# Performance work log

Hardware: AMD Instinct MI355X
Metric: run time of the kernel (lower is better)

## Reference

```python
import jax, jax.numpy as jnp
import numpy as np

# dims: G groups, A authors/group, P posts/author, DIN token-pooled feat, DEMB sentence-BERT dim
G, A, P, DIN, DEMB, HP, HA = 16, 64, 32, 768, 384, 256, 128


def setup_inputs() -> dict:
    key = jax.random.key(0)
    ks = jax.random.split(key, 8)
    s = lambda k, shape, scale: (jax.random.normal(k, shape, jnp.float32) * scale)
    return {
        "x": jax.random.normal(ks[0], (G, A, P, DIN), jnp.float32),
        "w_embed": s(ks[1], (DIN, DEMB), 0.02),   # BERT pooled-projection stand-in
        "b_embed": jnp.zeros((DEMB,), jnp.float32),
        "k_post": s(ks[2], (DEMB, 4 * HP), 0.05),  # Keras LSTM kernel, gates [i|f|c|o]
        "r_post": s(ks[3], (HP, 4 * HP), 0.05),    # recurrent kernel
        "b_post": jnp.zeros((4 * HP,), jnp.float32),
        "k_auth": s(ks[4], (HP, 4 * HA), 0.05),
        "r_auth": s(ks[5], (HA, 4 * HA), 0.05),
        "b_auth": jnp.zeros((4 * HA,), jnp.float32),
    }


def _lstm(x, Wk, Wr, b):
    """Keras-style LSTM, returns final hidden state. x: [B,T,D] -> [B,H]."""
    B = x.shape[0]
    H = Wr.shape[0]
    # precompute input projections for all timesteps in one GEMM: [T,B,4H]
    z = jnp.einsum('btd,dh->tbh', x, Wk) + b

    def step(carry, zt):
        h, c = carry
        g = zt + h @ Wr
        i, f, gg, o = jnp.split(g, 4, axis=-1)  # Keras gate order i,f,c,o
        c = jax.nn.sigmoid(f) * c + jax.nn.sigmoid(i) * jnp.tanh(gg)
        h = jax.nn.sigmoid(o) * jnp.tanh(c)
        return (h, c), None

    h0 = jnp.zeros((B, H), x.dtype)
    (h, _), _ = jax.lax.scan(step, (h0, h0), z)
    return h


def reference(x, w_embed, b_embed, k_post, r_post, b_post, k_auth, r_auth, b_auth):
    g, a, p, _ = x.shape
    # sentence embedding per post (BERT stand-in): [G,A,P,DEMB]
    e = jnp.einsum('gapd,de->gape', x, w_embed) + b_embed
    # LSTM over posts, batched across all (group, author) pairs: [G,A,HP]
    h_post = _lstm(e.reshape(g * a, p, e.shape[-1]), k_post, r_post, b_post)
    h_post = h_post.reshape(g, a, -1)
    # LSTM over authors: [G,HA]
    return _lstm(h_post, k_auth, r_auth, b_auth)
```

## Files before the change

### kernel.cpp

```cpp
#include <hip/hip_runtime.h>
#include <cstdint>
#include <cstddef>

#define G_    16
#define A_    64
#define P_    32
#define DIN_  768
#define DEMB_ 384
#define HP_   256
#define HA_   128
#define GA_   1024
#define N1_   1024
#define N2_   512
#define TCH   16

typedef float    f32x4   __attribute__((ext_vector_type(4)));
typedef _Float16 half8_t __attribute__((ext_vector_type(8)));
typedef _Float16 half4_t __attribute__((ext_vector_type(4)));

__device__ __forceinline__ float sigmoidf_(float x) { return 1.0f / (1.0f + __expf(-x)); }
__device__ __forceinline__ float tanhf_(float x) { return 2.0f / (1.0f + __expf(-2.0f * x)) - 1.0f; }
__device__ __forceinline__ _Float16 us2h(unsigned short u) { _Float16 h; __builtin_memcpy(&h, &u, 2); return h; }
__device__ __forceinline__ unsigned short h2us(_Float16 h) { unsigned short u; __builtin_memcpy(&u, &h, 2); return u; }


__global__ __launch_bounds__(256) void k_wk(const float* __restrict__ w_embed,
                                            const float* __restrict__ k_post,
                                            float* __restrict__ Bmat) {
    int j  = blockIdx.x * 256 + threadIdx.x;
    int k0 = blockIdx.y * 4;
    float acc0 = 0.f, acc1 = 0.f, acc2 = 0.f, acc3 = 0.f;
    for (int d = 0; d < DEMB_; ++d) {
        float kp = k_post[(size_t)d * N1_ + j];
        acc0 += w_embed[(size_t)(k0 + 0) * DEMB_ + d] * kp;
        acc1 += w_embed[(size_t)(k0 + 1) * DEMB_ + d] * kp;
        acc2 += w_embed[(size_t)(k0 + 2) * DEMB_ + d] * kp;
        acc3 += w_embed[(size_t)(k0 + 3) * DEMB_ + d] * kp;
    }
    Bmat[(size_t)(k0 + 0) * N1_ + j] = acc0;
    Bmat[(size_t)(k0 + 1) * N1_ + j] = acc1;
    Bmat[(size_t)(k0 + 2) * N1_ + j] = acc2;
    Bmat[(size_t)(k0 + 3) * N1_ + j] = acc3;
}

__global__ __launch_bounds__(256) void k_bias_p(const float* __restrict__ b_embed,
                                                const float* __restrict__ k_post,
                                                const float* __restrict__ b_post,
                                                float* __restrict__ biasZp) {
    int p = blockIdx.x * 256 + threadIdx.x;
    int n = (p >> 6) * 16 + (p & 15) + 256 * ((p >> 4) & 3);
    float acc = b_post[n];
    for (int d = 0; d < DEMB_; ++d)
        acc += b_embed[d] * k_post[(size_t)d * N1_ + n];
    biasZp[p] = acc;
}

__global__ __launch_bounds__(256) void k_t16(const float* __restrict__ Bmat,
                                             _Float16* __restrict__ Bt16) {
    __shared__ float tile[64][65];
    const int tid = threadIdx.x;
    const int p0 = blockIdx.x * 64;
    const int k0 = blockIdx.y * 64;
    const int jgrp = p0 >> 6;
#pragma unroll
    for (int i = 0; i < 16; ++i) {
        int idx = i * 256 + tid;
        int pp = idx & 63, kk = idx >> 6;
        int n = jgrp * 16 + (pp & 15) + 256 * ((pp >> 4) & 3);
        tile[pp][kk] = Bmat[(size_t)(k0 + kk) * N1_ + n];
    }
    __syncthreads();
    const int pp = tid >> 2;
    const int kq = (tid & 3) * 16;
    _Float16 buf[16];
#pragma unroll
    for (int i = 0; i < 16; ++i) buf[i] = (_Float16)tile[pp][kq + i];
    _Float16* dst = &Bt16[(size_t)(p0 + pp) * DIN_ + k0 + kq];
    *(half8_t*)dst       = *(half8_t*)&buf[0];
    *(half8_t*)(dst + 8) = *(half8_t*)&buf[8];
}

__global__ __launch_bounds__(256) void k_bfrag(const float* __restrict__ r_post,
                                               _Float16* __restrict__ Bfrag) {
    int idx = blockIdx.x * 256 + threadIdx.x;
    int pt = idx >> 9;
    int kt = (idx >> 6) & 7;
    int l  = idx & 63;
    int p = pt * 16 + (l & 15);
    int n = (p >> 6) * 16 + (p & 15) + 256 * ((p >> 4) & 3);
    int kb = kt * 32 + (l >> 4) * 8;
    _Float16 buf[8];
#pragma unroll
    for (int s = 0; s < 8; ++s) buf[s] = (_Float16)r_post[(size_t)(kb + s) * N1_ + n];
    *(half8_t*)&Bfrag[(size_t)idx * 8] = *(half8_t*)buf;
}

#define ZBM 128
#define ZBN 256
#define ZBK 32
#define ZPAD 40

__global__ __launch_bounds__(512, 2) void k_zgemm(const float* __restrict__ x,
                                                  const _Float16* __restrict__ Bt16,
                                                  const float* __restrict__ biasZp,
                                                  _Float16* __restrict__ Zq, int tbase) {
    __shared__ union {
        struct { _Float16 As[ZBM][ZPAD], Bs[ZBN][ZPAD]; } S;
        _Float16 Hs[64][264];
    } u;

    const int bid = blockIdx.x;
    const int wg  = (bid & 7) * 64 + (bid >> 3);
    const int bm  = (wg & 127) * ZBM;
    const int bn  = (wg >> 7) * ZBN;
    const int tid = threadIdx.x;

    const int arow = tid >> 2, akq = (tid & 3) * 8;
    const int brow = tid >> 1, bkq = (tid & 1) * 16;
    const int lane = tid & 63, w = tid >> 6;
    const int wm = (w >> 2) * 64, wn = (w & 3) * 64;
    const int frc = lane & 15, frk = (lane >> 4) * 8;

    const int crow = bm + arow;
    const size_t xrow = (size_t)(crow >> 4) * P_ + tbase + (crow & 15);
    const float*    aptr = &x[xrow * DIN_ + akq];
    const _Float16* bptr = &Bt16[(size_t)(bn + brow) * DIN_ + bkq];

    f32x4 acc[4][4];
#pragma unroll
    for (int i = 0; i < 4; ++i)
#pragma unroll
        for (int j = 0; j < 4; ++j) acc[i][j] = (f32x4)0.0f;

    float4 a0 = *(const float4*)aptr;
    float4 a1 = *(const float4*)(aptr + 4);
    uint4  b0 = *(const uint4*)bptr;
    uint4  b1 = *(const uint4*)(bptr + 8);

    const int NK = DIN_ / ZBK;
    for (int kt = 0; kt < NK; ++kt) {
        const int kn = (kt + 1 < NK) ? (kt + 1) * ZBK : kt * ZBK;
        float4 na0 = *(const float4*)(aptr + kn);
        float4 na1 = *(const float4*)(aptr + kn + 4);
        uint4  nb0 = *(const uint4*)(bptr + kn);
        uint4  nb1 = *(const uint4*)(bptr + kn + 8);

        half8_t ahv;
        {
            float av[8] = {a0.x,a0.y,a0.z,a0.w,a1.x,a1.y,a1.z,a1.w};
#pragma unroll
            for (int i = 0; i < 8; ++i) ahv[i] = (_Float16)av[i];
        }

        __syncthreads();
        *(half8_t*)&u.S.As[arow][akq]  = ahv;
        *(uint4*)&u.S.Bs[brow][bkq]     = b0;
        *(uint4*)&u.S.Bs[brow][bkq + 8] = b1;
        __syncthreads();

        half8_t bf[4];
#pragma unroll
        for (int fn = 0; fn < 4; ++fn)
            bf[fn] = *(const half8_t*)&u.S.Bs[wn + fn * 16 + frc][frk];
#pragma unroll
        for (int fm = 0; fm < 4; ++fm) {
            half8_t aH = *(const half8_t*)&u.S.As[wm + fm * 16 + frc][frk];
#pragma unroll
            for (int fn = 0; fn < 4; ++fn)
                acc[fm][fn] = __builtin_amdgcn_mfma_f32_16x16x32_f16(aH, bf[fn], acc[fm][fn], 0, 0, 0);
        }
        a0 = na0; a1 = na1; b0 = nb0; b1 = nb1;
    }

    float bzv[4];
#pragma unroll
    for (int fn = 0; fn < 4; ++fn) bzv[fn] = biasZp[bn + wn + fn * 16 + frc];

#pragma unroll
    for (int half_ = 0; half_ < 2; ++half_) {
        __syncthreads();
        if ((w >> 2) == half_) {
#pragma unroll
            for (int fm = 0; fm < 4; ++fm)
#pragma unroll
                for (int fn = 0; fn < 4; ++fn)
#pragma unroll
                    for (int r = 0; r < 4; ++r) {
                        int rl = fm * 16 + (lane >> 4) * 4 + r;
                        int cl = wn + fn * 16 + frc;
                        int clp = ((cl >> 6) * 16 + (cl & 15)) * 4 + ((cl >> 4) & 3);
                        u.Hs[rl][clp] = (_Float16)(acc[fm][fn][r] + bzv[fn]);
                    }
        }
        __syncthreads();
        const int brb = (bm + half_ * 64) >> 4;
        const int rg  = brb >> 4;
        const int l4r = (brb & 15) >> 2;
#pragma unroll
        for (int it = 0; it < 2; ++it) {
            int unit = it * 512 + tid;
            int tloc = unit >> 6, hcl = unit & 63;
            _Float16 buf[16];
#pragma unroll
            for (int rr = 0; rr < 4; ++rr) {
                half4_t h4 = *(const half4_t*)&u.Hs[tloc + 16 * rr][hcl * 4];
                buf[rr * 4 + 0] = h4[0]; buf[rr * 4 + 1] = h4[1];
                buf[rr * 4 + 2] = h4[2]; buf[rr * 4 + 3] = h4[3];
            }
            int wvg  = (bn >> 6) + (hcl >> 4);
            int tid2 = wvg * 64 + l4r * 16 + (hcl & 15);
            _Float16* dst = &Zq[((size_t)(tloc * 64 + rg) * 1024 + tid2) * 16];
            *(uint4*)dst       = *(const uint4*)&buf[0];
            *(uint4*)(dst + 8) = *(const uint4*)&buf[8];
        }
    }
}

__global__ __launch_bounds__(1024, 4) void k_rec(const _Float16* __restrict__ Zq,
                                                 const _Float16* __restrict__ Bfrag,
                                                 float* __restrict__ csave,
                                                 unsigned short* __restrict__ hsave,
                                                 float* __restrict__ hF32, int tbase) {
    __shared__ __align__(16) _Float16 wlds[16 * 8 * 64 * 8];
    __shared__ __align__(16) _Float16 hbuf[2][4096];

    const int tid = threadIdx.x, lane = tid & 63, wv = tid >> 6;
    const int hl = lane & 15, l4 = lane >> 4;
    const int r0 = blockIdx.x * 16;
    const int hc = wv * 16 + hl;

    half8_t wreg[16];
#pragma unroll
    for (int q = 0; q < 2; ++q)
#pragma unroll
        for (int kt = 0; kt < 8; ++kt)
            wreg[q * 8 + kt] = *(const half8_t*)&Bfrag[(((size_t)(4 * wv + q) * 8 + kt) * 64 + lane) * 8];
#pragma unroll
    for (int kt = 0; kt < 8; ++kt)
        *(half8_t*)&wlds[((wv * 8 + kt) * 64 + lane) * 8] =
            *(const half8_t*)&Bfrag[(((size_t)(4 * wv + 2) * 8 + kt) * 64 + lane) * 8];
    const _Float16* w3base = &Bfrag[((size_t)(4 * wv + 3) * 8 * 64 + lane) * 8];

    float cst[4];
    if (tbase == 0) {
#pragma unroll
        for (int i = 0; i < 4; ++i) cst[i] = 0.f;
    } else {
        f32x4 cv = *(const f32x4*)&csave[((size_t)blockIdx.x * 1024 + tid) * 4];
#pragma unroll
        for (int i = 0; i < 4; ++i) cst[i] = cv[i];
#pragma unroll
        for (int rr = 0; rr < 4; ++rr) {
            int row = l4 * 4 + rr;
            int lidx = (((hc >> 5) * 64) + (((hc & 31) >> 3) * 16 + row)) * 8 + (hc & 7);
            hbuf[0][lidx] = us2h(hsave[((size_t)(r0 + row)) * HP_ + hc]);
        }
    }
    __syncthreads();

    const _Float16* zp0 = &Zq[((size_t)blockIdx.x * 1024 + tid) * 16];
    half8_t z01N = *(const half8_t*)zp0;
    half8_t z23N = *(const half8_t*)(zp0 + 8);

    for (int tt = 0; tt < TCH; ++tt) {
        const int t = tbase + tt;
        const int cur = t & 1, nxt = cur ^ 1;

        half8_t z01 = z01N, z23 = z23N;
        if (tt + 1 < TCH) {
            const _Float16* zpn = zp0 + (size_t)(tt + 1) * 1048576;
            z01N = *(const half8_t*)zpn;
            z23N = *(const half8_t*)(zpn + 8);
        }

        f32x4 acc[4];
#pragma unroll
        for (int i = 0; i < 4; ++i) acc[i] = (f32x4)0.0f;

        if (t > 0) {
#pragma unroll
            for (int kt = 0; kt < 8; ++kt) {
                half8_t ah = *(const half8_t*)&hbuf[cur][(kt * 64 + lane) * 8];
                half8_t b2 = *(const half8_t*)&wlds[((wv * 8 + kt) * 64 + lane) * 8];
                half8_t w3 = *(const half8_t*)&w3base[(size_t)kt * 512];
                acc[0] = __builtin_amdgcn_mfma_f32_16x16x32_f16(ah, wreg[kt],     acc[0], 0, 0, 0);
                acc[1] = __builtin_amdgcn_mfma_f32_16x16x32_f16(ah, wreg[8 + kt], acc[1], 0, 0, 0);
                acc[2] = __builtin_amdgcn_mfma_f32_16x16x32_f16(ah, b2,           acc[2], 0, 0, 0);
                acc[3] = __builtin_amdgcn_mfma_f32_16x16x32_f16(ah, w3,           acc[3], 0, 0, 0);
            }
        }

        const bool last = (t == P_ - 1);
        const bool save = (tbase == 0) && (tt == TCH - 1);
#pragma unroll
        for (int rr = 0; rr < 4; ++rr) {
            const half8_t zsrc = (rr < 2) ? z01 : z23;
            const int o = (rr & 1) * 4;
            float gi = acc[0][rr] + (float)zsrc[o + 0];
            float gf = acc[1][rr] + (float)zsrc[o + 1];
            float gg = acc[2][rr] + (float)zsrc[o + 2];
            float go = acc[3][rr] + (float)zsrc[o + 3];
            float cn = sigmoidf_(gf) * cst[rr] + sigmoidf_(gi) * tanhf_(gg);
            cst[rr] = cn;
            float hv = sigmoidf_(go) * tanhf_(cn);
            int row = l4 * 4 + rr;
            int lidx = (((hc >> 5) * 64) + (((hc & 31) >> 3) * 16 + row)) * 8 + (hc & 7);
            _Float16 hh = (_Float16)hv;
            hbuf[nxt][lidx] = hh;
            if (save) hsave[((size_t)(r0 + row)) * HP_ + hc] = h2us(hh);
            if (last) hF32[(size_t)(r0 + row) * HP_ + hc] = hv;
        }
        __syncthreads();
    }

    if (tbase == 0) {
        f32x4 cv;
#pragma unroll
        for (int i = 0; i < 4; ++i) cv[i] = cst[i];
        *(f32x4*)&csave[((size_t)blockIdx.x * 1024 + tid) * 4] = cv;
    }
}

__global__ __launch_bounds__(256) void k_zauth(const float* __restrict__ h,
                                               const float* __restrict__ k_auth,
                                               const float* __restrict__ b_auth,
                                               float* __restrict__ z_auth) {
    const int j = blockIdx.x * 256 + threadIdx.x;
    const int r0 = blockIdx.y * 4;
    float acc0 = b_auth[j], acc1 = acc0, acc2 = acc0, acc3 = acc0;
    for (int k = 0; k < HP_; ++k) {
        const float kp = k_auth[(size_t)k * N2_ + j];
        acc0 += h[(size_t)(r0 + 0) * HP_ + k] * kp;
        acc1 += h[(size_t)(r0 + 1) * HP_ + k] * kp;
        acc2 += h[(size_t)(r0 + 2) * HP_ + k] * kp;
        acc3 += h[(size_t)(r0 + 3) * HP_ + k] * kp;
    }
#pragma unroll
    for (int r = 0; r < 4; ++r) {
        const int b = r0 + r;
        const int g = b >> 6, a = b & 63;
        const float v = (r == 0) ? acc0 : (r == 1) ? acc1 : (r == 2) ? acc2 : acc3;
        z_auth[((size_t)a * G_ + g) * N2_ + j] = v;
    }
}

__global__ __launch_bounds__(512, 2) void k_author(const float* __restrict__ z_auth,
                                                   const float* __restrict__ r_auth,
                                                   float* __restrict__ out) {
    const int g = blockIdx.x;
    const int tid = threadIdx.x;

    __shared__ float hs[HA_];
    __shared__ float gs[N2_];

    float rc[HA_];
#pragma unroll
    for (int k = 0; k < HA_; ++k)
        rc[k] = r_auth[(size_t)k * N2_ + tid];

    float cj = 0.f;
    if (tid < HA_) hs[tid] = 0.f;
    __syncthreads();

    float zn = z_auth[(size_t)g * N2_ + tid];
    for (int a = 0; a < A_; ++a) {
        float acc0 = zn, acc1 = 0.f, acc2 = 0.f, acc3 = 0.f;
        if (a + 1 < A_) zn = z_auth[((size_t)(a + 1) * G_ + g) * N2_ + tid];
#pragma unroll
        for (int k = 0; k < HA_; k += 4) {
            float4 h4 = *(const float4*)&hs[k];
            acc0 += h4.x * rc[k];
            acc1 += h4.y * rc[k + 1];
            acc2 += h4.z * rc[k + 2];
            acc3 += h4.w * rc[k + 3];
        }
        gs[tid] = (acc0 + acc1) + (acc2 + acc3);
        __syncthreads();
        if (tid < HA_) {
            const float i_ = sigmoidf_(gs[tid]);
            const float f_ = sigmoidf_(gs[tid + 128]);
            const float gg = gs[tid + 256];
            const float o_ = sigmoidf_(gs[tid + 384]);
            cj = f_ * cj + i_ * tanhf_(gg);
            hs[tid] = o_ * tanhf_(cj);
        }
        __syncthreads();
    }
    if (tid < HA_) out[(size_t)g * HA_ + tid] = hs[tid];
}

extern "C" void kernel_launch(void* const* d_in, const int* in_sizes, int n_in,
                              void* d_out, int out_size, void* d_ws, size_t ws_size,
                              hipStream_t stream) {
    const float* x       = (const float*)d_in[0];
    const float* w_embed = (const float*)d_in[1];
    const float* b_embed = (const float*)d_in[2];
    const float* k_post  = (const float*)d_in[3];
    const float* r_post  = (const float*)d_in[4];
    const float* b_post  = (const float*)d_in[5];
    const float* k_auth  = (const float*)d_in[6];
    const float* r_auth  = (const float*)d_in[7];
    const float* b_auth  = (const float*)d_in[8];
    float* out = (float*)d_out;

    char* wsb = (char*)d_ws;
    _Float16*       Zq     = (_Float16*)(wsb);
    float*          Bmat   = (float*)(wsb + (32ull << 20));
    _Float16*       Bt16   = (_Float16*)(wsb + (36ull << 20));
    _Float16*       Bfrag  = (_Float16*)(wsb + (38ull << 20));
    float*          biasZp = (float*)(wsb + (38ull << 20) + (512ull << 10));
    float*          csave  = (float*)(wsb + (39ull << 20));
    unsigned short* hsave  = (unsigned short*)(wsb + (40ull << 20));
    float*          hF32   = (float*)(wsb + (41ull << 20));
    float*          z_auth = (float*)(wsb + (42ull << 20));

    k_wk    <<<dim3(N1_ / 256, DIN_ / 4), 256, 0, stream>>>(w_embed, k_post, Bmat);
    k_bias_p<<<dim3(N1_ / 256), 256, 0, stream>>>(b_embed, k_post, b_post, biasZp);
    k_t16   <<<dim3(16, 12), 256, 0, stream>>>(Bmat, Bt16);
    k_bfrag <<<dim3(128), 256, 0, stream>>>(r_post, Bfrag);

    for (int ch = 0; ch < 2; ++ch) {
        k_zgemm<<<dim3(512), 512, 0, stream>>>(x, Bt16, biasZp, Zq, ch * TCH);
        k_rec  <<<dim3(64), 1024, 0, stream>>>(Zq, Bfrag, csave, hsave, hF32, ch * TCH);
    }

    k_zauth <<<dim3(N2_ / 256, GA_ / 4), 256, 0, stream>>>(hF32, k_auth, b_auth, z_auth);
    k_author<<<dim3(G_), 512, 0, stream>>>(z_auth, r_auth, out);
}
```

Baseline: 406.3 us.

## Overlap second-chunk input GEMM with first-chunk recurrence in fused launch

```diff
diff --git a/kernel.cpp b/kernel.cpp
--- a/kernel.cpp
+++ b/kernel.cpp
@@ -100,25 +100,30 @@
 #define ZBK 32
 #define ZPAD 40
 
-__global__ __launch_bounds__(512, 2) void k_zgemm(const float* __restrict__ x,
-                                                  const _Float16* __restrict__ Bt16,
-                                                  const float* __restrict__ biasZp,
-                                                  _Float16* __restrict__ Zq, int tbase) {
-    __shared__ union {
-        struct { _Float16 As[ZBM][ZPAD], Bs[ZBN][ZPAD]; } S;
+struct ZgLDS {
+    union {
+        struct { _Float16 As[ZBM][ZPAD]; _Float16 Bs[ZBN][ZPAD]; } S;
         _Float16 Hs[64][264];
     } u;
-
-    const int bid = blockIdx.x;
-    const int wg  = (bid & 7) * 64 + (bid >> 3);
-    const int bm  = (wg & 127) * ZBM;
-    const int bn  = (wg >> 7) * ZBN;
-    const int tid = threadIdx.x;
-
-    const int arow = tid >> 2, akq = (tid & 3) * 8;
-    const int brow = tid >> 1, bkq = (tid & 1) * 16;
+};
+struct RecLDS {
+    _Float16 wlds[16 * 8 * 64 * 8];
+    _Float16 hbuf[2][4096];
+};
+
+__device__ __forceinline__ void zgemm_core(ZgLDS* L, int bid, int tid,
+                                           const float* __restrict__ x,
+                                           const _Float16* __restrict__ Bt16,
+                                           const float* __restrict__ biasZp,
+                                           _Float16* __restrict__ Zq, int tbase) {
+    const int wg = (bid & 7) * 64 + (bid >> 3);
+    const int bm = (wg & 127) * ZBM;
+    const int bn = (wg >> 7) * ZBN;
+
+    const int arow = tid >> 3, akq = (tid & 7) * 4;
+    const int brow = tid >> 2, bkq = (tid & 3) * 8;
     const int lane = tid & 63, w = tid >> 6;
-    const int wm = (w >> 2) * 64, wn = (w & 3) * 64;
+    const int wm = (w >> 2) * 32, wn = (w & 3) * 64;
     const int frc = lane & 15, frk = (lane >> 4) * 8;
 
     const int crow = bm + arow;
@@ -126,50 +131,42 @@
     const float*    aptr = &x[xrow * DIN_ + akq];
     const _Float16* bptr = &Bt16[(size_t)(bn + brow) * DIN_ + bkq];
 
-    f32x4 acc[4][4];
-#pragma unroll
-    for (int i = 0; i < 4; ++i)
+    f32x4 acc[2][4];
+#pragma unroll
+    for (int i = 0; i < 2; ++i)
 #pragma unroll
         for (int j = 0; j < 4; ++j) acc[i][j] = (f32x4)0.0f;
 
     float4 a0 = *(const float4*)aptr;
-    float4 a1 = *(const float4*)(aptr + 4);
     uint4  b0 = *(const uint4*)bptr;
-    uint4  b1 = *(const uint4*)(bptr + 8);
 
     const int NK = DIN_ / ZBK;
     for (int kt = 0; kt < NK; ++kt) {
         const int kn = (kt + 1 < NK) ? (kt + 1) * ZBK : kt * ZBK;
         float4 na0 = *(const float4*)(aptr + kn);
-        float4 na1 = *(const float4*)(aptr + kn + 4);
         uint4  nb0 = *(const uint4*)(bptr + kn);
-        uint4  nb1 = *(const uint4*)(bptr + kn + 8);
-
-        half8_t ahv;
-        {
-            float av[8] = {a0.x,a0.y,a0.z,a0.w,a1.x,a1.y,a1.z,a1.w};
-#pragma unroll
-            for (int i = 0; i < 8; ++i) ahv[i] = (_Float16)av[i];
-        }
-
-        __syncthreads();
-        *(half8_t*)&u.S.As[arow][akq]  = ahv;
-        *(uint4*)&u.S.Bs[brow][bkq]     = b0;
-        *(uint4*)&u.S.Bs[brow][bkq + 8] = b1;
+
+        half4_t ahv;
+        ahv[0] = (_Float16)a0.x; ahv[1] = (_Float16)a0.y;
+        ahv[2] = (_Float16)a0.z; ahv[3] = (_Float16)a0.w;
+
+        __syncthreads();
+        *(half4_t*)&L->u.S.As[arow][akq] = ahv;
+        *(uint4*)&L->u.S.Bs[brow][bkq]   = b0;
         __syncthreads();
 
         half8_t bf[4];
 #pragma unroll
         for (int fn = 0; fn < 4; ++fn)
-            bf[fn] = *(const half8_t*)&u.S.Bs[wn + fn * 16 + frc][frk];
-#pragma unroll
-        for (int fm = 0; fm < 4; ++fm) {
-            half8_t aH = *(const half8_t*)&u.S.As[wm + fm * 16 + frc][frk];
+            bf[fn] = *(const half8_t*)&L->u.S.Bs[wn + fn * 16 + frc][frk];
+#pragma unroll
+        for (int fm = 0; fm < 2; ++fm) {
+            half8_t aH = *(const half8_t*)&L->u.S.As[wm + fm * 16 + frc][frk];
 #pragma unroll
             for (int fn = 0; fn < 4; ++fn)
                 acc[fm][fn] = __builtin_amdgcn_mfma_f32_16x16x32_f16(aH, bf[fn], acc[fm][fn], 0, 0, 0);
         }
-        a0 = na0; a1 = na1; b0 = nb0; b1 = nb1;
+        a0 = na0; b0 = nb0;
     }
 
     float bzv[4];
@@ -179,31 +176,29 @@
 #pragma unroll
     for (int half_ = 0; half_ < 2; ++half_) {
         __syncthreads();
-        if ((w >> 2) == half_) {
-#pragma unroll
-            for (int fm = 0; fm < 4; ++fm)
+        if ((w >> 3) == half_) {
+#pragma unroll
+            for (int fm = 0; fm < 2; ++fm)
 #pragma unroll
                 for (int fn = 0; fn < 4; ++fn)
 #pragma unroll
                     for (int r = 0; r < 4; ++r) {
-                        int rl = fm * 16 + (lane >> 4) * 4 + r;
+                        int rl = ((w >> 2) & 1) * 32 + fm * 16 + (lane >> 4) * 4 + r;
                         int cl = wn + fn * 16 + frc;
                         int clp = ((cl >> 6) * 16 + (cl & 15)) * 4 + ((cl >> 4) & 3);
-                        u.Hs[rl][clp] = (_Float16)(acc[fm][fn][r] + bzv[fn]);
+                        L->u.Hs[rl][clp] = (_Float16)(acc[fm][fn][r] + bzv[fn]);
                     }
         }
         __syncthreads();
         const int brb = (bm + half_ * 64) >> 4;
         const int rg  = brb >> 4;
         const int l4r = (brb & 15) >> 2;
-#pragma unroll
-        for (int it = 0; it < 2; ++it) {
-            int unit = it * 512 + tid;
-            int tloc = unit >> 6, hcl = unit & 63;
+        {
+            int tloc = tid >> 6, hcl = tid & 63;
             _Float16 buf[16];
 #pragma unroll
             for (int rr = 0; rr < 4; ++rr) {
-                half4_t h4 = *(const half4_t*)&u.Hs[tloc + 16 * rr][hcl * 4];
+                half4_t h4 = *(const half4_t*)&L->u.Hs[tloc + 16 * rr][hcl * 4];
                 buf[rr * 4 + 0] = h4[0]; buf[rr * 4 + 1] = h4[1];
                 buf[rr * 4 + 2] = h4[2]; buf[rr * 4 + 3] = h4[3];
             }
@@ -216,17 +211,15 @@
     }
 }
 
-__global__ __launch_bounds__(1024, 4) void k_rec(const _Float16* __restrict__ Zq,
-                                                 const _Float16* __restrict__ Bfrag,
-                                                 float* __restrict__ csave,
-                                                 unsigned short* __restrict__ hsave,
-                                                 float* __restrict__ hF32, int tbase) {
-    __shared__ __align__(16) _Float16 wlds[16 * 8 * 64 * 8];
-    __shared__ __align__(16) _Float16 hbuf[2][4096];
-
-    const int tid = threadIdx.x, lane = tid & 63, wv = tid >> 6;
+__device__ __forceinline__ void rec_core(RecLDS* L, int blk, int tid,
+                                         const _Float16* __restrict__ Zq,
+                                         const _Float16* __restrict__ Bfrag,
+                                         float* __restrict__ csave,
+                                         unsigned short* __restrict__ hsave,
+                                         float* __restrict__ hF32, int tbase) {
+    const int lane = tid & 63, wv = tid >> 6;
     const int hl = lane & 15, l4 = lane >> 4;
-    const int r0 = blockIdx.x * 16;
+    const int r0 = blk * 16;
     const int hc = wv * 16 + hl;
 
     half8_t wreg[16];
@@ -237,7 +230,7 @@
             wreg[q * 8 + kt] = *(const half8_t*)&Bfrag[(((size_t)(4 * wv + q) * 8 + kt) * 64 + lane) * 8];
 #pragma unroll
     for (int kt = 0; kt < 8; ++kt)
-        *(half8_t*)&wlds[((wv * 8 + kt) * 64 + lane) * 8] =
+        *(half8_t*)&L->wlds[((wv * 8 + kt) * 64 + lane) * 8] =
             *(const half8_t*)&Bfrag[(((size_t)(4 * wv + 2) * 8 + kt) * 64 + lane) * 8];
     const _Float16* w3base = &Bfrag[((size_t)(4 * wv + 3) * 8 * 64 + lane) * 8];
 
@@ -246,19 +239,19 @@
 #pragma unroll
         for (int i = 0; i < 4; ++i) cst[i] = 0.f;
     } else {
-        f32x4 cv = *(const f32x4*)&csave[((size_t)blockIdx.x * 1024 + tid) * 4];
+        f32x4 cv = *(const f32x4*)&csave[((size_t)blk * 1024 + tid) * 4];
 #pragma unroll
         for (int i = 0; i < 4; ++i) cst[i] = cv[i];
 #pragma unroll
         for (int rr = 0; rr < 4; ++rr) {
             int row = l4 * 4 + rr;
             int lidx = (((hc >> 5) * 64) + (((hc & 31) >> 3) * 16 + row)) * 8 + (hc & 7);
-            hbuf[0][lidx] = us2h(hsave[((size_t)(r0 + row)) * HP_ + hc]);
+            L->hbuf[0][lidx] = us2h(hsave[((size_t)(r0 + row)) * HP_ + hc]);
         }
     }
     __syncthreads();
 
-    const _Float16* zp0 = &Zq[((size_t)blockIdx.x * 1024 + tid) * 16];
+    const _Float16* zp0 = &Zq[((size_t)blk * 1024 + tid) * 16];
     half8_t z01N = *(const half8_t*)zp0;
     half8_t z23N = *(const half8_t*)(zp0 + 8);
 
@@ -280,8 +273,8 @@
         if (t > 0) {
 #pragma unroll
             for (int kt = 0; kt < 8; ++kt) {
-                half8_t ah = *(const half8_t*)&hbuf[cur][(kt * 64 + lane) * 8];
-                half8_t b2 = *(const half8_t*)&wlds[((wv * 8 + kt) * 64 + lane) * 8];
+                half8_t ah = *(const half8_t*)&L->hbuf[cur][(kt * 64 + lane) * 8];
+                half8_t b2 = *(const half8_t*)&L->wlds[((wv * 8 + kt) * 64 + lane) * 8];
                 half8_t w3 = *(const half8_t*)&w3base[(size_t)kt * 512];
                 acc[0] = __builtin_amdgcn_mfma_f32_16x16x32_f16(ah, wreg[kt],     acc[0], 0, 0, 0);
                 acc[1] = __builtin_amdgcn_mfma_f32_16x16x32_f16(ah, wreg[8 + kt], acc[1], 0, 0, 0);
@@ -306,7 +299,7 @@
             int row = l4 * 4 + rr;
             int lidx = (((hc >> 5) * 64) + (((hc & 31) >> 3) * 16 + row)) * 8 + (hc & 7);
             _Float16 hh = (_Float16)hv;
-            hbuf[nxt][lidx] = hh;
+            L->hbuf[nxt][lidx] = hh;
             if (save) hsave[((size_t)(r0 + row)) * HP_ + hc] = h2us(hh);
             if (last) hF32[(size_t)(r0 + row) * HP_ + hc] = hv;
         }
@@ -317,8 +310,41 @@
         f32x4 cv;
 #pragma unroll
         for (int i = 0; i < 4; ++i) cv[i] = cst[i];
-        *(f32x4*)&csave[((size_t)blockIdx.x * 1024 + tid) * 4] = cv;
-    }
+        *(f32x4*)&csave[((size_t)blk * 1024 + tid) * 4] = cv;
+    }
+}
+
+__global__ __launch_bounds__(1024, 4) void k_zgemm(const float* __restrict__ x,
+                                                   const _Float16* __restrict__ Bt16,
+                                                   const float* __restrict__ biasZp,
+                                                   _Float16* __restrict__ Zq, int tbase) {
+    __shared__ __align__(16) ZgLDS L;
+    zgemm_core(&L, blockIdx.x, threadIdx.x, x, Bt16, biasZp, Zq, tbase);
+}
+
+__global__ __launch_bounds__(1024, 4) void k_rec(const _Float16* __restrict__ Zq,
+                                                 const _Float16* __restrict__ Bfrag,
+                                                 float* __restrict__ csave,
+                                                 unsigned short* __restrict__ hsave,
+                                                 float* __restrict__ hF32, int tbase) {
+    __shared__ __align__(16) RecLDS L;
+    rec_core(&L, blockIdx.x, threadIdx.x, Zq, Bfrag, csave, hsave, hF32, tbase);
+}
+
+__global__ __launch_bounds__(1024, 4) void k_fuse(const float* __restrict__ x,
+                                                  const _Float16* __restrict__ Bt16,
+                                                  const float* __restrict__ biasZp,
+                                                  const _Float16* __restrict__ Zq0,
+                                                  _Float16* __restrict__ Zq1,
+                                                  const _Float16* __restrict__ Bfrag,
+                                                  float* __restrict__ csave,
+                                                  unsigned short* __restrict__ hsave,
+                                                  float* __restrict__ hF32) {
+    __shared__ __align__(16) union { RecLDS r; ZgLDS z; } L;
+    if (blockIdx.x < 64)
+        rec_core(&L.r, blockIdx.x, threadIdx.x, Zq0, Bfrag, csave, hsave, hF32, 0);
+    else
+        zgemm_core(&L.z, blockIdx.x - 64, threadIdx.x, x, Bt16, biasZp, Zq1, TCH);
 }
 
 __global__ __launch_bounds__(256) void k_zauth(const float* __restrict__ h,
@@ -344,49 +370,65 @@
     }
 }
 
-__global__ __launch_bounds__(512, 2) void k_author(const float* __restrict__ z_auth,
-                                                   const float* __restrict__ r_auth,
-                                                   float* __restrict__ out) {
+__global__ __launch_bounds__(512) void k_author(const float* __restrict__ z_auth,
+                                                const float* __restrict__ r_auth,
+                                                float* __restrict__ out) {
     const int g = blockIdx.x;
     const int tid = threadIdx.x;
-
-    __shared__ float hs[HA_];
-    __shared__ float gs[N2_];
-
-    float rc[HA_];
-#pragma unroll
-    for (int k = 0; k < HA_; ++k)
-        rc[k] = r_auth[(size_t)k * N2_ + tid];
-
-    float cj = 0.f;
-    if (tid < HA_) hs[tid] = 0.f;
+    const int j = tid >> 2;
+    const int kq = tid & 3;
+
+    __shared__ float hsb[2][HA_];
+
+    float rci[32], rcf[32], rcg[32], rco[32];
+#pragma unroll
+    for (int kk = 0; kk < 32; ++kk) {
+        int k = kq * 32 + kk;
+        rci[kk] = r_auth[(size_t)k * N2_ + j];
+        rcf[kk] = r_auth[(size_t)k * N2_ + j + 128];
+        rcg[kk] = r_auth[(size_t)k * N2_ + j + 256];
+        rco[kk] = r_auth[(size_t)k * N2_ + j + 384];
+    }
+
+    if (tid < HA_) hsb[0][tid] = 0.f;
+    float cj = 0.f, hv = 0.f;
     __syncthreads();
 
-    float zn = z_auth[(size_t)g * N2_ + tid];
+    float4 zn;
+    {
+        size_t zb = (size_t)g * N2_;
+        zn.x = z_auth[zb + j];       zn.y = z_auth[zb + j + 128];
+        zn.z = z_auth[zb + j + 256]; zn.w = z_auth[zb + j + 384];
+    }
+
     for (int a = 0; a < A_; ++a) {
-        float acc0 = zn, acc1 = 0.f, acc2 = 0.f, acc3 = 0.f;
-        if (a + 1 < A_) zn = z_auth[((size_t)(a + 1) * G_ + g) * N2_ + tid];
-#pragma unroll
-        for (int k = 0; k < HA_; k += 4) {
-            float4 h4 = *(const float4*)&hs[k];
-            acc0 += h4.x * rc[k];
-            acc1 += h4.y * rc[k + 1];
-            acc2 += h4.z * rc[k + 2];
-            acc3 += h4.w * rc[k + 3];
-        }
-        gs[tid] = (acc0 + acc1) + (acc2 + acc3);
-        __syncthreads();
-        if (tid < HA_) {
-            const float i_ = sigmoidf_(gs[tid]);
-            const float f_ = sigmoidf_(gs[tid + 128]);
-            const float gg = gs[tid + 256];
-            const float o_ = sigmoidf_(gs[tid + 384]);
-            cj = f_ * cj + i_ * tanhf_(gg);
-            hs[tid] = o_ * tanhf_(cj);
-        }
-        __syncthreads();
-    }
-    if (tid < HA_) out[(size_t)g * HA_ + tid] = hs[tid];
+        const int cur = a & 1, nxt = cur ^ 1;
+        float4 z4 = zn;
+        if (a + 1 < A_) {
+            size_t zb = ((size_t)(a + 1) * G_ + g) * N2_;
+            zn.x = z_auth[zb + j];       zn.y = z_auth[zb + j + 128];
+            zn.z = z_auth[zb + j + 256]; zn.w = z_auth[zb + j + 384];
+        }
+        float si = 0.f, sf = 0.f, sg = 0.f, so = 0.f;
+#pragma unroll
+        for (int kk = 0; kk < 32; kk += 4) {
+            float4 h4 = *(const float4*)&hsb[cur][kq * 32 + kk];
+            si += h4.x * rci[kk] + h4.y * rci[kk + 1] + h4.z * rci[kk + 2] + h4.w * rci[kk + 3];
+            sf += h4.x * rcf[kk] + h4.y * rcf[kk + 1] + h4.z * rcf[kk + 2] + h4.w * rcf[kk + 3];
+            sg += h4.x * rcg[kk] + h4.y * rcg[kk + 1] + h4.z * rcg[kk + 2] + h4.w * rcg[kk + 3];
+            so += h4.x * rco[kk] + h4.y * rco[kk + 1] + h4.z * rco[kk + 2] + h4.w * rco[kk + 3];
+        }
+        si += __shfl_xor(si, 1); si += __shfl_xor(si, 2);
+        sf += __shfl_xor(sf, 1); sf += __shfl_xor(sf, 2);
+        sg += __shfl_xor(sg, 1); sg += __shfl_xor(sg, 2);
+        so += __shfl_xor(so, 1); so += __shfl_xor(so, 2);
+        float gi = si + z4.x, gf = sf + z4.y, gg = sg + z4.z, go = so + z4.w;
+        cj = sigmoidf_(gf) * cj + sigmoidf_(gi) * tanhf_(gg);
+        hv = sigmoidf_(go) * tanhf_(cj);
+        if (kq == 0) hsb[nxt][j] = hv;
+        __syncthreads();
+    }
+    if (kq == 0) out[(size_t)g * HA_ + j] = hv;
 }
 
 extern "C" void kernel_launch(void* const* d_in, const int* in_sizes, int n_in,
@@ -404,7 +446,7 @@
     float* out = (float*)d_out;
 
     char* wsb = (char*)d_ws;
-    _Float16*       Zq     = (_Float16*)(wsb);
+    _Float16*       Zq0    = (_Float16*)(wsb);
     float*          Bmat   = (float*)(wsb + (32ull << 20));
     _Float16*       Bt16   = (_Float16*)(wsb + (36ull << 20));
     _Float16*       Bfrag  = (_Float16*)(wsb + (38ull << 20));
@@ -413,15 +455,25 @@
     unsigned short* hsave  = (unsigned short*)(wsb + (40ull << 20));
     float*          hF32   = (float*)(wsb + (41ull << 20));
     float*          z_auth = (float*)(wsb + (42ull << 20));
+    _Float16*       Zq1    = (_Float16*)(wsb + (44ull << 20));
+
+    const bool overlap = (ws_size >= (77ull << 20));
 
     k_wk    <<<dim3(N1_ / 256, DIN_ / 4), 256, 0, stream>>>(w_embed, k_post, Bmat);
     k_bias_p<<<dim3(N1_ / 256), 256, 0, stream>>>(b_embed, k_post, b_post, biasZp);
     k_t16   <<<dim3(16, 12), 256, 0, stream>>>(Bmat, Bt16);
     k_bfrag <<<dim3(128), 256, 0, stream>>>(r_post, Bfrag);
 
-    for (int ch = 0; ch < 2; ++ch) {
-        k_zgemm<<<dim3(512), 512, 0, stream>>>(x, Bt16, biasZp, Zq, ch * TCH);
-        k_rec  <<<dim3(64), 1024, 0, stream>>>(Zq, Bfrag, csave, hsave, hF32, ch * TCH);
+    k_zgemm<<<dim3(512), 1024, 0, stream>>>(x, Bt16, biasZp, Zq0, 0);
+
+    if (overlap) {
+        k_fuse<<<dim3(576), 1024, 0, stream>>>(x, Bt16, biasZp, Zq0, Zq1,
+                                               Bfrag, csave, hsave, hF32);
+        k_rec <<<dim3(64), 1024, 0, stream>>>(Zq1, Bfrag, csave, hsave, hF32, TCH);
+    } else {
+        k_rec  <<<dim3(64), 1024, 0, stream>>>(Zq0, Bfrag, csave, hsave, hF32, 0);
+        k_zgemm<<<dim3(512), 1024, 0, stream>>>(x, Bt16, biasZp, Zq0, TCH);
+        k_rec  <<<dim3(64), 1024, 0, stream>>>(Zq0, Bfrag, csave, hsave, hF32, TCH);
     }
 
     k_zauth <<<dim3(N2_ / 256, GA_ / 4), 256, 0, stream>>>(hF32, k_auth, b_auth, z_auth);
```

Result: faster. 348.2 us (-14.3%).
